# Kernel optimization log

Measured on AMD Instinct MI355X. Metric: run time of the kernel, lower is better.

The kernel has to match this reference:

```python
import jax, jax.numpy as jnp
import numpy as np

N_NODES = 50000


def gcn_conv(x, W, b, src, dst, num_nodes):
    # GCNConv (PyG defaults): h = D^{-1/2} (A + I) D^{-1/2} x W + b
    h = x @ W  # [N, out_dim]
    deg = jax.ops.segment_sum(jnp.ones(src.shape[0], h.dtype), dst, num_segments=num_nodes)
    dinv = jnp.where(deg > 0, jax.lax.rsqrt(deg), 0.0)
    norm = dinv[src] * dinv[dst]  # [E]
    out = jax.ops.segment_sum(h[src] * norm[:, None], dst, num_segments=num_nodes)
    return out + b


def setup_inputs() -> dict:
    key = jax.random.key(0)
    k1, k2, k3, k4 = jax.random.split(key, 4)
    x = jax.random.normal(k1, (N_NODES, 512), dtype=jnp.float32)
    ei = jax.random.randint(k2, (2, 800000), 0, N_NODES, dtype=jnp.int64)
    # Glorot-like init for GCN linear weights; PyG bias init zeros
    W1 = jax.random.normal(k3, (512, 128), dtype=jnp.float32) * (1.0 / np.sqrt(512))
    b1 = jnp.zeros((128,), dtype=jnp.float32)
    W2 = jax.random.normal(k4, (128, 64), dtype=jnp.float32) * (1.0 / np.sqrt(128))
    b2 = jnp.zeros((64,), dtype=jnp.float32)
    return {"x": x, "ei": ei, "W1": W1, "b1": b1, "W2": W2, "b2": b2}


def reference(x, ei, W1, b1, W2, b2):
    n = x.shape[0]
    loops = jnp.arange(n, dtype=ei.dtype)
    src = jnp.concatenate([ei[0], loops])  # add self-loops (PyG default)
    dst = jnp.concatenate([ei[1], loops])
    h = jax.nn.relu(gcn_conv(x, W1, b1, src, dst, n))
    return jax.nn.relu(gcn_conv(h, W2, b2, src, dst, n))
```

## Files before the change

kernel.cpp:

```cpp
#include <hip/hip_runtime.h>


#define N_FEAT0 512
#define N_FEAT1 128
#define N_FEAT2 64
#define SLACK 64

typedef _Float16 f16x8 __attribute__((ext_vector_type(8)));
typedef float f32x16 __attribute__((ext_vector_type(16)));


__global__ void k_prep(const float* __restrict__ W1, const float* __restrict__ W2,
                       _Float16* __restrict__ Wt, _Float16* __restrict__ Wt2,
                       int* __restrict__ cnt, int n) {
    int idx = blockIdx.x * 256 + threadIdx.x;
    if (idx < 65536) {
        int k = idx >> 7;
        int c = idx & 127;
        Wt[(size_t)c * 512 + k] = (_Float16)W1[idx];
    } else if (idx < 65536 + 8192) {
        int j = idx - 65536;
        int k = j >> 6;
        int c = j & 63;
        Wt2[(size_t)c * 128 + k] = (_Float16)W2[j];
    }
    if (idx < n) cnt[idx] = 0;
}


__global__ void k_count_scatter(const int* __restrict__ src, const int* __restrict__ dst,
                                int* __restrict__ cnt, int* __restrict__ srcs_pad, int E) {
    int i = blockIdx.x * blockDim.x + threadIdx.x;
    int stride = gridDim.x * blockDim.x;
    for (; i < E; i += stride) {
        int d = dst[i];
        int p = atomicAdd(&cnt[d], 1);
        if (p < SLACK) srcs_pad[(size_t)d * SLACK + p] = src[i];
    }
}

__global__ __launch_bounds__(256) void k_gemm1_mfma(const float* __restrict__ X,
                                                    const _Float16* __restrict__ Wt,
                                                    const int* __restrict__ cnt,
                                                    _Float16* __restrict__ H, int n) {
    __shared__ __align__(16) _Float16 ah[4][64][8];
    __shared__ __align__(16) _Float16 wh[4][128][8];
    const int tid = threadIdx.x;
    const int lane = tid & 63;
    const int w = tid >> 6;
    const int row0 = blockIdx.x * 64;

    f32x16 acc0 = {}, acc1 = {};

    const int arow = tid >> 2;
    const int aoct = tid & 3;
    const int gr = row0 + arow;
    const float* xrow = X + (size_t)gr * N_FEAT0 + aoct * 8;

    const int u0 = tid,        c0 = u0 >> 2, o0 = u0 & 3;
    const int u1 = tid + 256,  c1 = u1 >> 2, o1 = u1 & 3;
    const _Float16* wp0 = Wt + (size_t)c0 * 512 + o0 * 8;
    const _Float16* wp1 = Wt + (size_t)c1 * 512 + o1 * 8;

    float4 xa, xb;
    f16x8 w0r, w1r;
    if (gr < n) {
        xa = ((const float4*)xrow)[0];
        xb = ((const float4*)xrow)[1];
    } else {
        xa = xb = make_float4(0.f, 0.f, 0.f, 0.f);
    }
    w0r = *(const f16x8*)wp0;
    w1r = *(const f16x8*)wp1;

    for (int k0 = 0; k0 < N_FEAT0; k0 += 32) {
        f16x8 hv;
        hv[0] = (_Float16)xa.x; hv[1] = (_Float16)xa.y;
        hv[2] = (_Float16)xa.z; hv[3] = (_Float16)xa.w;
        hv[4] = (_Float16)xb.x; hv[5] = (_Float16)xb.y;
        hv[6] = (_Float16)xb.z; hv[7] = (_Float16)xb.w;
        *(f16x8*)(&ah[aoct][arow][0]) = hv;
        *(f16x8*)(&wh[o0][c0][0]) = w0r;
        *(f16x8*)(&wh[o1][c1][0]) = w1r;
        __syncthreads();

        const int k1 = k0 + 32;
        if (k1 < N_FEAT0) {
            if (gr < n) {
                xa = ((const float4*)(xrow + k1))[0];
                xb = ((const float4*)(xrow + k1))[1];
            } else {
                xa = xb = make_float4(0.f, 0.f, 0.f, 0.f);
            }
            w0r = *(const f16x8*)(wp0 + k1);
            w1r = *(const f16x8*)(wp1 + k1);
        }

#pragma unroll
        for (int kb = 0; kb < 2; kb++) {
            const int oct = kb * 2 + (lane >> 5);
            f16x8 a0 = *(const f16x8*)(&ah[oct][(lane & 31)][0]);
            f16x8 a1 = *(const f16x8*)(&ah[oct][32 + (lane & 31)][0]);
            f16x8 b  = *(const f16x8*)(&wh[oct][w * 32 + (lane & 31)][0]);
            acc0 = __builtin_amdgcn_mfma_f32_32x32x16_f16(a0, b, acc0, 0, 0, 0);
            acc1 = __builtin_amdgcn_mfma_f32_32x32x16_f16(a1, b, acc1, 0, 0, 0);
        }
        __syncthreads();
    }

    const int col = w * 32 + (lane & 31);
#pragma unroll
    for (int rq = 0; rq < 4; rq++)
#pragma unroll
        for (int rr = 0; rr < 4; rr++) {
            const int reg = rq * 4 + rr;
            const int r_base = rr + 8 * rq + 4 * (lane >> 5);
            int row = row0 + r_base;
            if (row < n) {
                float di = rsqrtf((float)(cnt[row] + 1));
                H[(size_t)row * N_FEAT1 + col] = (_Float16)(acc0[reg] * di);
            }
            row = row0 + 32 + r_base;
            if (row < n) {
                float di = rsqrtf((float)(cnt[row] + 1));
                H[(size_t)row * N_FEAT1 + col] = (_Float16)(acc1[reg] * di);
            }
        }
}

__global__ __launch_bounds__(256) void k_gemm2_mfma(const _Float16* __restrict__ A,
                                                    const _Float16* __restrict__ Wt2,
                                                    const int* __restrict__ cnt,
                                                    _Float16* __restrict__ H2, int n) {
    __shared__ __align__(16) _Float16 ah[16][128][8];
    __shared__ __align__(16) _Float16 bh[16][64][8];
    const int tid = threadIdx.x;
    const int lane = tid & 63;
    const int w = tid >> 6;
    const int row0 = blockIdx.x * 128;

#pragma unroll
    for (int it = 0; it < 8; it++) {
        int u = tid + it * 256;
        int r = u >> 4;
        int o = u & 15;
        int gr = row0 + r;
        f16x8 v = {};
        if (gr < n) v = *(const f16x8*)(A + (size_t)gr * 128 + o * 8);
        *(f16x8*)(&ah[o][r][0]) = v;
    }
#pragma unroll
    for (int it = 0; it < 4; it++) {
        int u = tid + it * 256;
        int c = u >> 4;
        int o = u & 15;
        *(f16x8*)(&bh[o][c][0]) = *(const f16x8*)(Wt2 + (size_t)c * 128 + o * 8);
    }
    __syncthreads();

    f32x16 acc0 = {}, acc1 = {};
#pragma unroll
    for (int s = 0; s < 8; s++) {
        const int oct = s * 2 + (lane >> 5);
        f16x8 a  = *(const f16x8*)(&ah[oct][w * 32 + (lane & 31)][0]);
        f16x8 b0 = *(const f16x8*)(&bh[oct][(lane & 31)][0]);
        f16x8 b1 = *(const f16x8*)(&bh[oct][32 + (lane & 31)][0]);
        acc0 = __builtin_amdgcn_mfma_f32_32x32x16_f16(a, b0, acc0, 0, 0, 0);
        acc1 = __builtin_amdgcn_mfma_f32_32x32x16_f16(a, b1, acc1, 0, 0, 0);
    }

#pragma unroll
    for (int rq = 0; rq < 4; rq++)
#pragma unroll
        for (int rr = 0; rr < 4; rr++) {
            const int row = row0 + w * 32 + rr + 8 * rq + 4 * (lane >> 5);
            if (row < n) {
                const float di = rsqrtf((float)(cnt[row] + 1));
                const int reg = rq * 4 + rr;
                H2[(size_t)row * N_FEAT2 + (lane & 31)] = (_Float16)(acc0[reg] * di);
                H2[(size_t)row * N_FEAT2 + 32 + (lane & 31)] = (_Float16)(acc1[reg] * di);
            }
        }
}


__global__ __launch_bounds__(256) void k_gather128(const int* __restrict__ srcs_pad,
                                                   const int* __restrict__ cnt,
                                                   const _Float16* __restrict__ H,
                                                   const float* __restrict__ bias,
                                                   _Float16* __restrict__ out, int n) {
    const int node = blockIdx.x * 16 + (threadIdx.x >> 4);
    const int li = threadIdx.x & 15;
    if (node >= n) return;
    const f16x8* __restrict__ H8 = (const f16x8*)H;
    f16x8 sv = H8[(size_t)node * 16 + li];
    float a[8];
#pragma unroll
    for (int q = 0; q < 8; q++) a[q] = (float)sv[q];
    const int c = cnt[node];
    const float di = rsqrtf((float)(c + 1));
    const int e = c < SLACK ? c : SLACK;
    const int* __restrict__ sp = srcs_pad + (size_t)node * SLACK;
    int j = 0;
    for (; j + 3 < e; j += 4) {
        int s0 = sp[j], s1 = sp[j + 1], s2 = sp[j + 2], s3 = sp[j + 3];
        f16x8 v0 = H8[(size_t)s0 * 16 + li];
        f16x8 v1 = H8[(size_t)s1 * 16 + li];
        f16x8 v2 = H8[(size_t)s2 * 16 + li];
        f16x8 v3 = H8[(size_t)s3 * 16 + li];
#pragma unroll
        for (int q = 0; q < 8; q++)
            a[q] += ((float)v0[q] + (float)v1[q]) + ((float)v2[q] + (float)v3[q]);
    }
    for (; j < e; j++) {
        f16x8 v0 = H8[(size_t)sp[j] * 16 + li];
#pragma unroll
        for (int q = 0; q < 8; q++) a[q] += (float)v0[q];
    }
    float4 b0 = *(const float4*)(bias + li * 8);
    float4 b1 = *(const float4*)(bias + li * 8 + 4);
    f16x8 r;
    r[0] = (_Float16)fmaxf(a[0] * di + b0.x, 0.f);
    r[1] = (_Float16)fmaxf(a[1] * di + b0.y, 0.f);
    r[2] = (_Float16)fmaxf(a[2] * di + b0.z, 0.f);
    r[3] = (_Float16)fmaxf(a[3] * di + b0.w, 0.f);
    r[4] = (_Float16)fmaxf(a[4] * di + b1.x, 0.f);
    r[5] = (_Float16)fmaxf(a[5] * di + b1.y, 0.f);
    r[6] = (_Float16)fmaxf(a[6] * di + b1.z, 0.f);
    r[7] = (_Float16)fmaxf(a[7] * di + b1.w, 0.f);
    ((f16x8*)out)[(size_t)node * 16 + li] = r;
}

__global__ __launch_bounds__(256) void k_gather64(const int* __restrict__ srcs_pad,
                                                  const int* __restrict__ cnt,
                                                  const _Float16* __restrict__ H,
                                                  const float* __restrict__ bias,
                                                  float* __restrict__ out, int n) {
    const int node = blockIdx.x * 32 + (threadIdx.x >> 3);
    const int li = threadIdx.x & 7;
    if (node >= n) return;
    const f16x8* __restrict__ H8 = (const f16x8*)H;
    f16x8 sv = H8[(size_t)node * 8 + li];
    float a[8];
#pragma unroll
    for (int q = 0; q < 8; q++) a[q] = (float)sv[q];
    const int c = cnt[node];
    const float di = rsqrtf((float)(c + 1));
    const int e = c < SLACK ? c : SLACK;
    const int* __restrict__ sp = srcs_pad + (size_t)node * SLACK;
    int j = 0;
    for (; j + 3 < e; j += 4) {
        int s0 = sp[j], s1 = sp[j + 1], s2 = sp[j + 2], s3 = sp[j + 3];
        f16x8 v0 = H8[(size_t)s0 * 8 + li];
        f16x8 v1 = H8[(size_t)s1 * 8 + li];
        f16x8 v2 = H8[(size_t)s2 * 8 + li];
        f16x8 v3 = H8[(size_t)s3 * 8 + li];
#pragma unroll
        for (int q = 0; q < 8; q++)
            a[q] += ((float)v0[q] + (float)v1[q]) + ((float)v2[q] + (float)v3[q]);
    }
    for (; j < e; j++) {
        f16x8 v0 = H8[(size_t)sp[j] * 8 + li];
#pragma unroll
        for (int q = 0; q < 8; q++) a[q] += (float)v0[q];
    }
    float4 b0 = *(const float4*)(bias + li * 8);
    float4 b1 = *(const float4*)(bias + li * 8 + 4);
    float4 r0, r1;
    r0.x = fmaxf(a[0] * di + b0.x, 0.f);
    r0.y = fmaxf(a[1] * di + b0.y, 0.f);
    r0.z = fmaxf(a[2] * di + b0.z, 0.f);
    r0.w = fmaxf(a[3] * di + b0.w, 0.f);
    r1.x = fmaxf(a[4] * di + b1.x, 0.f);
    r1.y = fmaxf(a[5] * di + b1.y, 0.f);
    r1.z = fmaxf(a[6] * di + b1.z, 0.f);
    r1.w = fmaxf(a[7] * di + b1.w, 0.f);
    float* op = out + (size_t)node * N_FEAT2 + li * 8;
    *(float4*)op = r0;
    *(float4*)(op + 4) = r1;
}


extern "C" void kernel_launch(void* const* d_in, const int* in_sizes, int n_in,
                              void* d_out, int out_size, void* d_ws, size_t ws_size,
                              hipStream_t stream) {
    const float* x  = (const float*)d_in[0];
    const int*   ei = (const int*)d_in[1];
    const float* W1 = (const float*)d_in[2];
    const float* b1 = (const float*)d_in[3];
    const float* W2 = (const float*)d_in[4];
    const float* b2 = (const float*)d_in[5];
    float* out = (float*)d_out;

    const int n = in_sizes[0] / N_FEAT0;
    const int E = in_sizes[1] / 2;
    const int* src = ei;
    const int* dst = ei + E;

    char* p = (char*)d_ws;
    _Float16* h16      = (_Float16*)p;
    _Float16* agg16    = (_Float16*)(p + 12800000);
    _Float16* h2_16    = (_Float16*)(p + 25600000);
    int*      cnt      = (int*)(p + 32000000);
    int*      srcs_pad = (int*)(p + 32200064);
    _Float16* Wt       = (_Float16*)(p + 45000064);
    _Float16* Wt2      = (_Float16*)(p + 45131136);

    const int B = 256;
    const int nprep = (65536 + 8192 > n ? 65536 + 8192 : n);

    k_prep<<<(nprep + B - 1) / B, B, 0, stream>>>(W1, W2, Wt, Wt2, cnt, n);
    k_count_scatter<<<(E + B - 1) / B, B, 0, stream>>>(src, dst, cnt, srcs_pad, E);

    k_gemm1_mfma<<<(n + 63) / 64, B, 0, stream>>>(x, Wt, cnt, h16, n);
    k_gather128<<<(n + 15) / 16, B, 0, stream>>>(srcs_pad, cnt, h16, b1, agg16, n);

    k_gemm2_mfma<<<(n + 127) / 128, B, 0, stream>>>(agg16, Wt2, cnt, h2_16, n);
    k_gather64<<<(n + 31) / 32, B, 0, stream>>>(srcs_pad, cnt, h2_16, b2, out, n);
}
```

Baseline: 145.1 us.

## Double-buffer GEMM1 LDS with 64-wide K steps and vectorize edge scatter

The first GEMM now stages 64-wide K slices into double-buffered shared memory, which removes one of the two barriers per iteration and halves the number of loop iterations. The edge count/scatter kernel is also changed so each thread loads four edges with int4 reads and issues four atomics. These changes target barrier overhead and load instruction count, in exchange for more shared memory and registers per block, which could lower occupancy.

```diff
diff --git a/kernel.cpp b/kernel.cpp
--- a/kernel.cpp
+++ b/kernel.cpp
@@ -30,12 +30,25 @@
 
 __global__ void k_count_scatter(const int* __restrict__ src, const int* __restrict__ dst,
                                 int* __restrict__ cnt, int* __restrict__ srcs_pad, int E) {
-    int i = blockIdx.x * blockDim.x + threadIdx.x;
-    int stride = gridDim.x * blockDim.x;
-    for (; i < E; i += stride) {
-        int d = dst[i];
-        int p = atomicAdd(&cnt[d], 1);
-        if (p < SLACK) srcs_pad[(size_t)d * SLACK + p] = src[i];
+    const int t = blockIdx.x * blockDim.x + threadIdx.x;
+    const int base = t * 4;
+    if (base + 3 < E) {
+        int4 d = *(const int4*)(dst + base);
+        int4 s = *(const int4*)(src + base);
+        int p0 = atomicAdd(&cnt[d.x], 1);
+        int p1 = atomicAdd(&cnt[d.y], 1);
+        int p2 = atomicAdd(&cnt[d.z], 1);
+        int p3 = atomicAdd(&cnt[d.w], 1);
+        if (p0 < SLACK) srcs_pad[(size_t)d.x * SLACK + p0] = s.x;
+        if (p1 < SLACK) srcs_pad[(size_t)d.y * SLACK + p1] = s.y;
+        if (p2 < SLACK) srcs_pad[(size_t)d.z * SLACK + p2] = s.z;
+        if (p3 < SLACK) srcs_pad[(size_t)d.w * SLACK + p3] = s.w;
+    } else {
+        for (int i = base; i < E; i++) {
+            int d = dst[i];
+            int p = atomicAdd(&cnt[d], 1);
+            if (p < SLACK) srcs_pad[(size_t)d * SLACK + p] = src[i];
+        }
     }
 }
 
@@ -43,8 +56,8 @@
                                                     const _Float16* __restrict__ Wt,
                                                     const int* __restrict__ cnt,
                                                     _Float16* __restrict__ H, int n) {
-    __shared__ __align__(16) _Float16 ah[4][64][8];
-    __shared__ __align__(16) _Float16 wh[4][128][8];
+    __shared__ __align__(16) _Float16 ah[2][8][64][8];
+    __shared__ __align__(16) _Float16 wh[2][8][128][8];
     const int tid = threadIdx.x;
     const int lane = tid & 63;
     const int w = tid >> 6;
@@ -52,60 +65,70 @@
 
     f32x16 acc0 = {}, acc1 = {};
 
-    const int arow = tid >> 2;
-    const int aoct = tid & 3;
-    const int gr = row0 + arow;
-    const float* xrow = X + (size_t)gr * N_FEAT0 + aoct * 8;
-
-    const int u0 = tid,        c0 = u0 >> 2, o0 = u0 & 3;
-    const int u1 = tid + 256,  c1 = u1 >> 2, o1 = u1 & 3;
-    const _Float16* wp0 = Wt + (size_t)c0 * 512 + o0 * 8;
-    const _Float16* wp1 = Wt + (size_t)c1 * 512 + o1 * 8;
-
-    float4 xa, xb;
-    f16x8 w0r, w1r;
-    if (gr < n) {
-        xa = ((const float4*)xrow)[0];
-        xb = ((const float4*)xrow)[1];
-    } else {
-        xa = xb = make_float4(0.f, 0.f, 0.f, 0.f);
-    }
-    w0r = *(const f16x8*)wp0;
-    w1r = *(const f16x8*)wp1;
-
-    for (int k0 = 0; k0 < N_FEAT0; k0 += 32) {
-        f16x8 hv;
-        hv[0] = (_Float16)xa.x; hv[1] = (_Float16)xa.y;
-        hv[2] = (_Float16)xa.z; hv[3] = (_Float16)xa.w;
-        hv[4] = (_Float16)xb.x; hv[5] = (_Float16)xb.y;
-        hv[6] = (_Float16)xb.z; hv[7] = (_Float16)xb.w;
-        *(f16x8*)(&ah[aoct][arow][0]) = hv;
-        *(f16x8*)(&wh[o0][c0][0]) = w0r;
-        *(f16x8*)(&wh[o1][c1][0]) = w1r;
+    const int arow = tid >> 3;
+    const int aoct = tid & 7;
+    const int gr0 = row0 + arow;
+    const int gr1 = row0 + arow + 32;
+    const float* xp0 = X + (size_t)gr0 * N_FEAT0 + aoct * 8;
+    const float* xp1 = X + (size_t)gr1 * N_FEAT0 + aoct * 8;
+    const _Float16* wp = Wt + (size_t)(tid >> 3) * 512 + aoct * 8;
+
+    float4 xa0, xb0, xa1, xb1;
+    f16x8 wr0, wr1, wr2, wr3;
+
+    {
+        const float4 z = make_float4(0.f, 0.f, 0.f, 0.f);
+        if (gr0 < n) { xa0 = ((const float4*)xp0)[0]; xb0 = ((const float4*)xp0)[1]; }
+        else { xa0 = z; xb0 = z; }
+        if (gr1 < n) { xa1 = ((const float4*)xp1)[0]; xb1 = ((const float4*)xp1)[1]; }
+        else { xa1 = z; xb1 = z; }
+        wr0 = *(const f16x8*)(wp);
+        wr1 = *(const f16x8*)(wp + 32 * 512);
+        wr2 = *(const f16x8*)(wp + 64 * 512);
+        wr3 = *(const f16x8*)(wp + 96 * 512);
+    }
+
+    for (int t = 0; t < 8; t++) {
+        const int buf = t & 1;
+        f16x8 h0, h1;
+        h0[0] = (_Float16)xa0.x; h0[1] = (_Float16)xa0.y;
+        h0[2] = (_Float16)xa0.z; h0[3] = (_Float16)xa0.w;
+        h0[4] = (_Float16)xb0.x; h0[5] = (_Float16)xb0.y;
+        h0[6] = (_Float16)xb0.z; h0[7] = (_Float16)xb0.w;
+        h1[0] = (_Float16)xa1.x; h1[1] = (_Float16)xa1.y;
+        h1[2] = (_Float16)xa1.z; h1[3] = (_Float16)xa1.w;
+        h1[4] = (_Float16)xb1.x; h1[5] = (_Float16)xb1.y;
+        h1[6] = (_Float16)xb1.z; h1[7] = (_Float16)xb1.w;
+        *(f16x8*)(&ah[buf][aoct][arow][0]) = h0;
+        *(f16x8*)(&ah[buf][aoct][arow + 32][0]) = h1;
+        *(f16x8*)(&wh[buf][aoct][(tid >> 3)][0]) = wr0;
+        *(f16x8*)(&wh[buf][aoct][(tid >> 3) + 32][0]) = wr1;
+        *(f16x8*)(&wh[buf][aoct][(tid >> 3) + 64][0]) = wr2;
+        *(f16x8*)(&wh[buf][aoct][(tid >> 3) + 96][0]) = wr3;
+
+        if (t < 7) {
+            const int k1 = (t + 1) * 64;
+            const float4 z = make_float4(0.f, 0.f, 0.f, 0.f);
+            if (gr0 < n) { xa0 = ((const float4*)(xp0 + k1))[0]; xb0 = ((const float4*)(xp0 + k1))[1]; }
+            else { xa0 = z; xb0 = z; }
+            if (gr1 < n) { xa1 = ((const float4*)(xp1 + k1))[0]; xb1 = ((const float4*)(xp1 + k1))[1]; }
+            else { xa1 = z; xb1 = z; }
+            wr0 = *(const f16x8*)(wp + k1);
+            wr1 = *(const f16x8*)(wp + 32 * 512 + k1);
+            wr2 = *(const f16x8*)(wp + 64 * 512 + k1);
+            wr3 = *(const f16x8*)(wp + 96 * 512 + k1);
+        }
         __syncthreads();
 
-        const int k1 = k0 + 32;
-        if (k1 < N_FEAT0) {
-            if (gr < n) {
-                xa = ((const float4*)(xrow + k1))[0];
-                xb = ((const float4*)(xrow + k1))[1];
-            } else {
-                xa = xb = make_float4(0.f, 0.f, 0.f, 0.f);
-            }
-            w0r = *(const f16x8*)(wp0 + k1);
-            w1r = *(const f16x8*)(wp1 + k1);
-        }
-
-#pragma unroll
-        for (int kb = 0; kb < 2; kb++) {
+#pragma unroll
+        for (int kb = 0; kb < 4; kb++) {
             const int oct = kb * 2 + (lane >> 5);
-            f16x8 a0 = *(const f16x8*)(&ah[oct][(lane & 31)][0]);
-            f16x8 a1 = *(const f16x8*)(&ah[oct][32 + (lane & 31)][0]);
-            f16x8 b  = *(const f16x8*)(&wh[oct][w * 32 + (lane & 31)][0]);
+            f16x8 a0 = *(const f16x8*)(&ah[buf][oct][(lane & 31)][0]);
+            f16x8 a1 = *(const f16x8*)(&ah[buf][oct][32 + (lane & 31)][0]);
+            f16x8 b  = *(const f16x8*)(&wh[buf][oct][w * 32 + (lane & 31)][0]);
             acc0 = __builtin_amdgcn_mfma_f32_32x32x16_f16(a0, b, acc0, 0, 0, 0);
             acc1 = __builtin_amdgcn_mfma_f32_32x32x16_f16(a1, b, acc1, 0, 0, 0);
         }
-        __syncthreads();
     }
 
     const int col = w * 32 + (lane & 31);
@@ -310,7 +333,7 @@
     const int nprep = (65536 + 8192 > n ? 65536 + 8192 : n);
 
     k_prep<<<(nprep + B - 1) / B, B, 0, stream>>>(W1, W2, Wt, Wt2, cnt, n);
-    k_count_scatter<<<(E + B - 1) / B, B, 0, stream>>>(src, dst, cnt, srcs_pad, E);
+    k_count_scatter<<<((E + 3) / 4 + B - 1) / B, B, 0, stream>>>(src, dst, cnt, srcs_pad, E);
 
     k_gemm1_mfma<<<(n + 63) / 64, B, 0, stream>>>(x, Wt, cnt, h16, n);
     k_gather128<<<(n + 15) / 16, B, 0, stream>>>(srcs_pad, cnt, h16, b1, agg16, n);
```

Result: slower. 162.1 us (+11.7%).
